# Performance work log

Measured on AMD Instinct MI355X. Metric: run time of the kernel, lower is better.

Reference implementation:

```python
import jax, jax.numpy as jnp
import numpy as np


def setup_inputs() -> dict:
    key = jax.random.key(0)
    k1, k2 = jax.random.split(key)
    img_render_points = jax.random.normal(k1, (128, 128, 2), dtype=jnp.float32)
    ref_catheter_contour_point_cloud = jax.random.normal(k2, (16384, 2), dtype=jnp.float32)
    return {
        "img_render_points": img_render_points,
        "ref_catheter_contour_point_cloud": ref_catheter_contour_point_cloud,
    }


def reference(img_render_points, ref_catheter_contour_point_cloud):
    # Flatten to point cloud (N, 2)
    pc = img_render_points.reshape(-1, 2)
    ref = ref_catheter_contour_point_cloud  # (M, 2)
    # Pairwise Euclidean distances (N, M); torch.norm(..., dim=2) equivalent
    diff = pc[:, None, :] - ref[None, :, :]          # (N, M, 2)
    distances = jnp.sqrt(jnp.sum(diff * diff, axis=-1))  # (N, M)
    min_d1 = jnp.min(distances, axis=1)  # nearest ref point for each render point
    min_d2 = jnp.min(distances, axis=0)  # nearest render point for each ref point
    chamfer_loss = jnp.sum(min_d1) + jnp.sum(min_d2)
    return chamfer_loss
```

## Files before the change

kernel.cpp:

```cpp
#include <hip/hip_runtime.h>
#include <math.h>

#define NPTS  16384
#define BLK   256
#define Q     8
#define QB    (NPTS / (BLK * Q))
#define TCH   64
#define CHUNK (NPTS / TCH)
#define U     (CHUNK / 2)


__global__ __launch_bounds__(BLK) void cc_min_kernel(
        const float2* __restrict__ pc,
        const float2* __restrict__ ref,
        unsigned int* __restrict__ ws,
        float* __restrict__ out) {
    __shared__ float4 sxy[U];
    __shared__ float2 sz[U];

    int b   = blockIdx.x;
    int dir = b / (QB * TCH);
    int rem = b % (QB * TCH);
    int qb  = rem / TCH;
    int ch  = rem % TCH;

    if (b == 0 && threadIdx.x == 0) out[0] = 0.0f;

    const float2* __restrict__ qry = dir ? ref : pc;
    const float2* __restrict__ tgt = dir ? pc  : ref;

    for (int u = threadIdx.x; u < U; u += BLK) {
        float4 t2 = ((const float4*)tgt)[ch * U + u];
        sxy[u] = make_float4(-2.0f * t2.x, -2.0f * t2.y,
                             -2.0f * t2.z, -2.0f * t2.w);
        sz[u] = make_float2(fmaf(t2.x, t2.x, t2.y * t2.y),
                            fmaf(t2.z, t2.z, t2.w * t2.w));
    }

    float px[Q], py[Q], pn[Q], m[Q];
    int qbase = qb * (BLK * Q) + threadIdx.x;
#pragma unroll
    for (int j = 0; j < Q; ++j) {
        float2 p = qry[qbase + j * BLK];
        px[j] = p.x;
        py[j] = p.y;
        pn[j] = fmaf(p.x, p.x, p.y * p.y);
        m[j]  = INFINITY;
    }
    __syncthreads();

#pragma unroll 4
    for (int u = 0; u < U; ++u) {
        float4 xy = sxy[u];
        float2 z  = sz[u];
#pragma unroll
        for (int j = 0; j < Q; ++j) {
            float s1 = fmaf(px[j], xy.x, fmaf(py[j], xy.y, z.x));
            float s2 = fmaf(px[j], xy.z, fmaf(py[j], xy.w, z.y));
            m[j] = fminf(fminf(m[j], s1), s2);
        }
    }

#pragma unroll
    for (int j = 0; j < Q; ++j) {
        float d2 = fmaxf(m[j] + pn[j], 0.0f);
        atomicMin(&ws[dir * NPTS + qbase + j * BLK], __float_as_uint(d2));
    }
}

__global__ __launch_bounds__(BLK) void cc_final_kernel(
        const unsigned int* __restrict__ ws, float* __restrict__ out) {
    int i = blockIdx.x * BLK + threadIdx.x;
    float s = 0.0f;
    for (int k = i; k < 2 * NPTS; k += gridDim.x * BLK)
        s += sqrtf(__uint_as_float(ws[k]));

#pragma unroll
    for (int off = 32; off > 0; off >>= 1)
        s += __shfl_down(s, off, 64);

    if ((threadIdx.x & 63) == 0)
        atomicAdd(out, s);
}

extern "C" void kernel_launch(void* const* d_in, const int* in_sizes, int n_in,
                              void* d_out, int out_size, void* d_ws, size_t ws_size,
                              hipStream_t stream) {
    const float2* pc  = (const float2*)d_in[0];
    const float2* ref = (const float2*)d_in[1];
    float* out = (float*)d_out;
    unsigned int* ws = (unsigned int*)d_ws;

    cc_min_kernel<<<2 * QB * TCH, BLK, 0, stream>>>(pc, ref, ws, out);
    cc_final_kernel<<<64, BLK, 0, stream>>>(ws, out);
}
```

Before: 87.52 us.

## Replace brute-force chamfer search with uniform-grid spatial binning nearest-neighbor query

Points from both clouds are first binned into a fixed 64x64 grid over [-5,5]^2, using per-cell atomic counters and a capped overflow list. Each wavefront then takes one cell's query points and searches outward in rings of cells, stopping once every lane's best distance is within the ring bound. Points in the overflow list are checked exhaustively. This swaps the O(N*M) all-pairs scan for a local neighborhood search. The cost is serial, data-dependent global loads, three kernel launches instead of two, and dependence on a fixed bounding box and fixed capacities.

```diff
diff --git a/kernel.cpp b/kernel.cpp
--- a/kernel.cpp
+++ b/kernel.cpp
@@ -1,86 +1,125 @@
 #include <hip/hip_runtime.h>
 #include <math.h>
 
-#define NPTS  16384
-#define BLK   256
-#define Q     8
-#define QB    (NPTS / (BLK * Q))
-#define TCH   64
-#define CHUNK (NPTS / TCH)
-#define U     (CHUNK / 2)
+#define NPTS 16384
+#define G    64
+#define NB   (G * G)
+#define CAP  128
+#define OCAP 2048
+#define BV   5.0f
+#define H    (2.0f * BV / G)
+#define INVH (1.0f / H)
 
 
-__global__ __launch_bounds__(BLK) void cc_min_kernel(
-        const float2* __restrict__ pc,
-        const float2* __restrict__ ref,
-        unsigned int* __restrict__ ws,
+__global__ __launch_bounds__(256) void k_zero(unsigned int* __restrict__ cnt,
+                                              float* __restrict__ out) {
+    int i = blockIdx.x * 256 + threadIdx.x;
+    if (i < 2 * NB + 2) cnt[i] = 0u;
+    if (i == 0) out[0] = 0.0f;
+}
+
+__global__ __launch_bounds__(256) void k_scatter(
+        const float2* __restrict__ pc, const float2* __restrict__ ref,
+        unsigned int* __restrict__ cnt, unsigned int* __restrict__ ovf_cnt,
+        float2* __restrict__ binned, float2* __restrict__ ovf) {
+    int t  = blockIdx.x * 256 + threadIdx.x;
+    int cl = t >> 14;
+    int i  = t & (NPTS - 1);
+    float2 p = (cl ? ref : pc)[i];
+    int bx = (int)floorf((p.x + BV) * INVH); bx = min(max(bx, 0), G - 1);
+    int by = (int)floorf((p.y + BV) * INVH); by = min(max(by, 0), G - 1);
+    int b = by * G + bx;
+    unsigned idx = atomicAdd(&cnt[cl * NB + b], 1u);
+    if (idx < CAP) {
+        binned[(cl * NB + b) * CAP + idx] = p;
+    } else {
+        unsigned oi = atomicAdd(&ovf_cnt[cl], 1u);
+        if (oi < OCAP) ovf[cl * OCAP + oi] = p;
+    }
+}
+
+__global__ __launch_bounds__(256) void k_query(
+        const float2* __restrict__ pc, const float2* __restrict__ ref,
+        const unsigned int* __restrict__ cnt, const unsigned int* __restrict__ ovf_cnt,
+        const float2* __restrict__ binned, const float2* __restrict__ ovf,
         float* __restrict__ out) {
-    __shared__ float4 sxy[U];
-    __shared__ float2 sz[U];
+    int d    = blockIdx.y;
+    int td   = 1 - d;
+    int w    = blockIdx.x * 4 + (threadIdx.x >> 6);
+    int lane = threadIdx.x & 63;
+    float sum = 0.0f;
 
-    int b   = blockIdx.x;
-    int dir = b / (QB * TCH);
-    int rem = b % (QB * TCH);
-    int qb  = rem / TCH;
-    int ch  = rem % TCH;
+    if (w < NB) {
+        int c  = w;
+        int cx = c & (G - 1), cy = c >> 6;
+        const unsigned int* tcnt = cnt + td * NB;
+        const float2* tbin = binned + (size_t)td * NB * CAP;
+        int nq = (int)min(cnt[d * NB + c], (unsigned)CAP);
+        unsigned novf = min(ovf_cnt[td], (unsigned)OCAP);
 
-    if (b == 0 && threadIdx.x == 0) out[0] = 0.0f;
+        for (int base = 0; base < nq; base += 64) {
+            bool valid = (base + lane) < nq;
+            float2 q = valid ? binned[((size_t)d * NB + c) * CAP + base + lane]
+                             : make_float2(0.0f, 0.0f);
+            float best = valid ? INFINITY : 0.0f;
 
-    const float2* __restrict__ qry = dir ? ref : pc;
-    const float2* __restrict__ tgt = dir ? pc  : ref;
+            for (unsigned j = 0; j < novf; ++j) {
+                float2 tp = ovf[td * OCAP + j];
+                float ddx = q.x - tp.x, ddy = q.y - tp.y;
+                best = fminf(best, fmaf(ddx, ddx, ddy * ddy));
+            }
 
-    for (int u = threadIdx.x; u < U; u += BLK) {
-        float4 t2 = ((const float4*)tgt)[ch * U + u];
-        sxy[u] = make_float4(-2.0f * t2.x, -2.0f * t2.y,
-                             -2.0f * t2.z, -2.0f * t2.w);
-        sz[u] = make_float2(fmaf(t2.x, t2.x, t2.y * t2.y),
-                            fmaf(t2.z, t2.z, t2.w * t2.w));
-    }
+            auto scan_cell = [&](int x, int y) {
+                if ((unsigned)x < G && (unsigned)y < G) {
+                    int t  = y * G + x;
+                    int tn = (int)min(tcnt[t], (unsigned)CAP);
+                    const float2* tp = tbin + (size_t)t * CAP;
+                    for (int j = 0; j < tn; ++j) {
+                        float2 pt = tp[j];
+                        float ddx = q.x - pt.x, ddy = q.y - pt.y;
+                        best = fminf(best, fmaf(ddx, ddx, ddy * ddy));
+                    }
+                }
+            };
 
-    float px[Q], py[Q], pn[Q], m[Q];
-    int qbase = qb * (BLK * Q) + threadIdx.x;
-#pragma unroll
-    for (int j = 0; j < Q; ++j) {
-        float2 p = qry[qbase + j * BLK];
-        px[j] = p.x;
-        py[j] = p.y;
-        pn[j] = fmaf(p.x, p.x, p.y * p.y);
-        m[j]  = INFINITY;
-    }
-    __syncthreads();
-
-#pragma unroll 4
-    for (int u = 0; u < U; ++u) {
-        float4 xy = sxy[u];
-        float2 z  = sz[u];
-#pragma unroll
-        for (int j = 0; j < Q; ++j) {
-            float s1 = fmaf(px[j], xy.x, fmaf(py[j], xy.y, z.x));
-            float s2 = fmaf(px[j], xy.z, fmaf(py[j], xy.w, z.y));
-            m[j] = fminf(fminf(m[j], s1), s2);
+            for (int r = 0; r < G; ++r) {
+                if (r == 0) {
+                    scan_cell(cx, cy);
+                } else {
+                    for (int dx = -r; dx <= r; ++dx) {
+                        scan_cell(cx + dx, cy - r);
+                        scan_cell(cx + dx, cy + r);
+                    }
+                    for (int dy = -r + 1; dy <= r - 1; ++dy) {
+                        scan_cell(cx - r, cy + dy);
+                        scan_cell(cx + r, cy + dy);
+                    }
+                }
+                float bound = (float)r * H;
+                if (__all(best <= bound * bound)) break;
+            }
+            if (valid) sum += sqrtf(best);
+        }
+    } else if (w == NB) {
+        unsigned n = min(ovf_cnt[d], (unsigned)OCAP);
+        const float2* tgt = d ? pc : ref;
+        for (unsigned i = lane; i < n; i += 64) {
+            float2 q = ovf[d * OCAP + i];
+            float best = INFINITY;
+            for (int j = 0; j < NPTS; ++j) {
+                float2 tp = tgt[j];
+                float ddx = q.x - tp.x, ddy = q.y - tp.y;
+                best = fminf(best, fmaf(ddx, ddx, ddy * ddy));
+            }
+            sum += sqrtf(best);
         }
     }
 
 #pragma unroll
-    for (int j = 0; j < Q; ++j) {
-        float d2 = fmaxf(m[j] + pn[j], 0.0f);
-        atomicMin(&ws[dir * NPTS + qbase + j * BLK], __float_as_uint(d2));
-    }
-}
-
-__global__ __launch_bounds__(BLK) void cc_final_kernel(
-        const unsigned int* __restrict__ ws, float* __restrict__ out) {
-    int i = blockIdx.x * BLK + threadIdx.x;
-    float s = 0.0f;
-    for (int k = i; k < 2 * NPTS; k += gridDim.x * BLK)
-        s += sqrtf(__uint_as_float(ws[k]));
-
-#pragma unroll
     for (int off = 32; off > 0; off >>= 1)
-        s += __shfl_down(s, off, 64);
-
-    if ((threadIdx.x & 63) == 0)
-        atomicAdd(out, s);
+        sum += __shfl_down(sum, off, 64);
+    if (lane == 0 && sum != 0.0f)
+        atomicAdd(out, sum);
 }
 
 extern "C" void kernel_launch(void* const* d_in, const int* in_sizes, int n_in,
@@ -89,8 +128,14 @@
     const float2* pc  = (const float2*)d_in[0];
     const float2* ref = (const float2*)d_in[1];
     float* out = (float*)d_out;
-    unsigned int* ws = (unsigned int*)d_ws;
 
-    cc_min_kernel<<<2 * QB * TCH, BLK, 0, stream>>>(pc, ref, ws, out);
-    cc_final_kernel<<<64, BLK, 0, stream>>>(ws, out);
+    char* w = (char*)d_ws;
+    unsigned int* cnt     = (unsigned int*)(w);
+    unsigned int* ovf_cnt = (unsigned int*)(w + 32768);
+    float2*       binned  = (float2*)(w + 65536);
+    float2*       ovf     = (float2*)(w + 65536 + (size_t)2 * NB * CAP * sizeof(float2));
+
+    k_zero<<<(2 * NB + 2 + 255) / 256, 256, 0, stream>>>(cnt, out);
+    k_scatter<<<(2 * NPTS) / 256, 256, 0, stream>>>(pc, ref, cnt, ovf_cnt, binned, ovf);
+    k_query<<<dim3(1025, 2), 256, 0, stream>>>(pc, ref, cnt, ovf_cnt, binned, ovf, out);
 }
```

Result: slower. 161.3 us (+84.3%).
